# Optimization experiments

Hardware: AMD Instinct MI355X
Metric: run time of the kernel (lower is better)

## Reference

```python
import jax, jax.numpy as jnp
import numpy as np

B, N, C = 8, 4096, 512
H = 8
OUT = 512
DH = C // H  # 64
LN_EPS = 1e-5
L2_EPS = 1e-12


def setup_inputs() -> dict:
    key = jax.random.key(0)
    ks = jax.random.split(key, 6)
    x = jax.random.normal(ks[0], (B, N, C), dtype=jnp.float32)
    ln_g = jnp.ones((C,), dtype=jnp.float32)
    ln_b = jnp.zeros((C,), dtype=jnp.float32)
    qkv_w = jax.random.normal(ks[1], (3 * C, C), dtype=jnp.float32) * 0.02  # torch Linear weight [out,in]
    temperature = jnp.ones((H, 1, 1), dtype=jnp.float32)
    proj_w = jax.random.normal(ks[2], (OUT, C), dtype=jnp.float32) * 0.02
    proj_b = jnp.zeros((OUT,), dtype=jnp.float32)
    return {"x": x, "ln_g": ln_g, "ln_b": ln_b, "qkv_w": qkv_w,
            "temperature": temperature, "proj_w": proj_w, "proj_b": proj_b}


def reference(x, ln_g, ln_b, qkv_w, temperature, proj_w, proj_b):
    # LayerNorm
    mu = jnp.mean(x, axis=-1, keepdims=True)
    var = jnp.mean(jnp.square(x - mu), axis=-1, keepdims=True)
    xn = (x - mu) * jax.lax.rsqrt(var + LN_EPS) * ln_g + ln_b
    # QKV projection (no bias)
    qkv = xn @ qkv_w.T  # [B,N,3C]
    qkv = qkv.reshape(B, N, 3, H, DH).transpose(2, 0, 3, 4, 1)  # [3,B,H,DH,N]
    q, k, v = qkv[0], qkv[1], qkv[2]  # each [B,H,DH,N] (already 'transposed' channel layout)
    # L2-normalize q,k along token dim (matches F.normalize eps behavior)
    q = q / jnp.clip(jnp.linalg.norm(q, axis=-1, keepdims=True), L2_EPS)
    k = k / jnp.clip(jnp.linalg.norm(k, axis=-1, keepdims=True), L2_EPS)
    # channel attention [B,H,DH,DH], scaled by per-head temperature
    attn = jnp.einsum('bhdn,bhen->bhde', q, k) * temperature[None]
    attn = jax.nn.softmax(attn, axis=-1)
    out = jnp.einsum('bhde,bhen->bhdn', attn, v)  # [B,H,DH,N]
    out = out.transpose(0, 3, 1, 2).reshape(B, N, H * DH)  # [B,N,C]
    out = jax.nn.gelu(out, approximate=False)
    out = out @ proj_w.T + proj_b
    return out
```

## Files before the change

kernel.cpp:

```cpp
#include <hip/hip_runtime.h>
#include <hip/hip_bf16.h>

typedef __hip_bfloat16 bf16;
typedef __bf16 bfrag __attribute__((ext_vector_type(8)));
typedef float f32x4 __attribute__((ext_vector_type(4)));

#define AS1 __attribute__((address_space(1)))
#define AS3 __attribute__((address_space(3)))

static constexpr int Bb = 8, Nn = 4096, Cc = 512, Hh = 8;
static constexpr int Mtok = Bb * Nn;
static constexpr int QKVC = 3 * Cc;
static constexpr size_t WS_NEED = 57147392;

__device__ __forceinline__ void gl_lds16(const void* g, void* l) {
  __builtin_amdgcn_global_load_lds((const AS1 void*)g, (AS3 void*)l, 16, 0, 0);
}
__device__ __forceinline__ float gelu_exact(float x) {
  return 0.5f * x * (1.0f + erff(x * 0.70710678118654752f));
}

__global__ __launch_bounds__(256) void fill_f32(float* o, float val, int n) {
  int i = blockIdx.x * 256 + threadIdx.x;
  if (i < n) o[i] = val;
}

__global__ __launch_bounds__(256) void cvt_f32_bf16(const float* __restrict__ a,
                                                    bf16* __restrict__ o, int n) {
  int i = (blockIdx.x * 256 + threadIdx.x) * 8;
  if (i + 8 <= n) {
    float f[8];
    *(float4*)f       = *(const float4*)(a + i);
    *(float4*)(f + 4) = *(const float4*)(a + i + 4);
    bf16 v[8];
#pragma unroll
    for (int j = 0; j < 8; ++j) v[j] = __float2bfloat16(f[j]);
    *(uint4*)(o + i) = *(uint4*)v;
  }
}

__global__ __launch_bounds__(256) void ln_kernel(const float* __restrict__ x,
                                                 const float* __restrict__ gw,
                                                 const float* __restrict__ bw,
                                                 bf16* __restrict__ xn) {
  int tok  = blockIdx.x * 4 + (threadIdx.x >> 6);
  int lane = threadIdx.x & 63;
  const float* xr = x + (size_t)tok * Cc + lane * 8;
  float f[8];
  *(float4*)f       = *(const float4*)xr;
  *(float4*)(f + 4) = *(const float4*)(xr + 4);
  float s = 0.f;
#pragma unroll
  for (int j = 0; j < 8; ++j) s += f[j];
#pragma unroll
  for (int m = 32; m; m >>= 1) s += __shfl_xor(s, m);
  float mu = s * (1.0f / 512.0f);
  float q = 0.f;
#pragma unroll
  for (int j = 0; j < 8; ++j) { float d = f[j] - mu; q += d * d; }
#pragma unroll
  for (int m = 32; m; m >>= 1) q += __shfl_xor(q, m);
  float rstd = rsqrtf(q * (1.0f / 512.0f) + 1e-5f);
  bf16 o[8];
#pragma unroll
  for (int j = 0; j < 8; ++j)
    o[j] = __float2bfloat16((f[j] - mu) * rstd * gw[lane * 8 + j] + bw[lane * 8 + j]);
  *(uint4*)(xn + (size_t)tok * Cc + lane * 8) = *(uint4*)o;
}

template <typename TC>
__global__ __launch_bounds__(256) void gemm_bt(const bf16* __restrict__ A,
                                               const bf16* __restrict__ B,
                                               TC* __restrict__ C,
                                               int M, int N, int K,
                                               const float* __restrict__ bias,
                                               long sA_z, long sB_z, long sC_z) {
  A += (size_t)blockIdx.z * sA_z;
  B += (size_t)blockIdx.z * sB_z;
  C += (size_t)blockIdx.z * sC_z;
  __shared__ __align__(16) bf16 smem[16384];
  bf16* sA = smem;
  bf16* sB = smem + 8192;
  int t = threadIdx.x, w = t >> 6, lane = t & 63, fr = lane & 15, quad = lane >> 4;
  int n0 = blockIdx.x * 128, m0 = blockIdx.y * 128;
  int wm = (w >> 1) * 64, wn = (w & 1) * 64;
  f32x4 acc[4][4] = {};

  for (int k0 = 0; k0 < K; k0 += 64) {
    __syncthreads();
#pragma unroll
    for (int c2 = 0; c2 < 4; ++c2) {
      int c = w * 4 + c2;
      int row = c * 8 + (lane >> 3);
      int ke  = (lane & 7) * 8;
      gl_lds16(A + (size_t)(m0 + row) * K + k0 + ke, (char*)sA + c * 1024);
      gl_lds16(B + (size_t)(n0 + row) * K + k0 + ke, (char*)sB + c * 1024);
    }
    __syncthreads();
#pragma unroll
    for (int kk = 0; kk < 64; kk += 32) {
      bfrag af[4], bg[4];
#pragma unroll
      for (int i = 0; i < 4; ++i) af[i] = *(const bfrag*)(sA + (wm + i * 16 + fr) * 64 + kk + quad * 8);
#pragma unroll
      for (int j = 0; j < 4; ++j) bg[j] = *(const bfrag*)(sB + (wn + j * 16 + fr) * 64 + kk + quad * 8);
#pragma unroll
      for (int i = 0; i < 4; ++i)
#pragma unroll
        for (int j = 0; j < 4; ++j)
          acc[i][j] = __builtin_amdgcn_mfma_f32_16x16x32_bf16(af[i], bg[j], acc[i][j], 0, 0, 0);
    }
  }

  if constexpr (__is_same(TC, float)) {
#pragma unroll
    for (int j = 0; j < 4; ++j) {
      float bj = bias ? bias[n0 + wn + j * 16 + fr] : 0.0f;
#pragma unroll
      for (int i = 0; i < 4; ++i)
#pragma unroll
        for (int r = 0; r < 4; ++r)
          C[(size_t)(m0 + wm + i * 16 + quad * 4 + r) * N + n0 + wn + j * 16 + fr] =
              acc[i][j][r] + bj;
    }
  } else {
    __syncthreads();
    bf16* ct = smem;
#pragma unroll
    for (int j = 0; j < 4; ++j) {
      float bj = bias ? bias[n0 + wn + j * 16 + fr] : 0.0f;
#pragma unroll
      for (int i = 0; i < 4; ++i)
#pragma unroll
        for (int r = 0; r < 4; ++r)
          ct[(wm + i * 16 + quad * 4 + r) * 128 + wn + j * 16 + fr] =
              __float2bfloat16(acc[i][j][r] + bj);
    }
    __syncthreads();
#pragma unroll
    for (int r8 = 0; r8 < 8; ++r8) {
      int row = r8 * 16 + (t >> 4);
      int ce  = (t & 15) * 8;
      *(uint4*)(C + (size_t)(m0 + row) * N + n0 + ce) = *(const uint4*)(smem + row * 128 + ce);
    }
  }
}

__global__ __launch_bounds__(256) void xtx(const bf16* __restrict__ xn,
                                           float* __restrict__ Gcov) {
  int tile = blockIdx.x;
  int split = blockIdx.y;
  int b = blockIdx.z;
  int m0 = (tile >> 2) * 128, n0 = (tile & 3) * 128;
  int t = threadIdx.x, w = t >> 6, lane = t & 63, fr = lane & 15, quad = lane >> 4;
  int wm = (w >> 1) * 64, wn = (w & 1) * 64;
  __shared__ __align__(16) bf16 sA[8192], sB[8192];
  f32x4 acc[4][4] = {};
  const bf16* xb = xn + ((size_t)b * Nn + split * 512) * Cc;
  int ch0 = (t & 15) * 8;
  int tg  = t >> 4;
  unsigned swz = (unsigned)(t & 7);
  unsigned wpos = (((unsigned)(tg >> 1) ^ swz) * 16u) + (unsigned)(tg & 1) * 8u;
  uint4 va[4], vb[4];
#pragma unroll
  for (int j = 0; j < 4; ++j) {
    int tk = tg * 4 + j;
    va[j] = *(const uint4*)(xb + (size_t)tk * Cc + m0 + ch0);
    vb[j] = *(const uint4*)(xb + (size_t)tk * Cc + n0 + ch0);
  }
  for (int kc = 0; kc < 8; ++kc) {
    __syncthreads();
#pragma unroll
    for (int k = 0; k < 4; ++k) {
      unsigned a0 = ((const unsigned*)&va[0])[k], a1 = ((const unsigned*)&va[1])[k];
      unsigned a2 = ((const unsigned*)&va[2])[k], a3 = ((const unsigned*)&va[3])[k];
      uint2 lo = { (a0 & 0xffffu) | (a1 << 16), (a2 & 0xffffu) | (a3 << 16) };
      uint2 hi = { (a0 >> 16) | (a1 & 0xffff0000u), (a2 >> 16) | (a3 & 0xffff0000u) };
      *(uint2*)((char*)sA + (unsigned)(ch0 + 2 * k) * 128 + wpos) = lo;
      *(uint2*)((char*)sA + (unsigned)(ch0 + 2 * k + 1) * 128 + wpos) = hi;
      unsigned b0 = ((const unsigned*)&vb[0])[k], b1 = ((const unsigned*)&vb[1])[k];
      unsigned b2 = ((const unsigned*)&vb[2])[k], b3 = ((const unsigned*)&vb[3])[k];
      uint2 lo2 = { (b0 & 0xffffu) | (b1 << 16), (b2 & 0xffffu) | (b3 << 16) };
      uint2 hi2 = { (b0 >> 16) | (b1 & 0xffff0000u), (b2 >> 16) | (b3 & 0xffff0000u) };
      *(uint2*)((char*)sB + (unsigned)(ch0 + 2 * k) * 128 + wpos) = lo2;
      *(uint2*)((char*)sB + (unsigned)(ch0 + 2 * k + 1) * 128 + wpos) = hi2;
    }
    __syncthreads();
    if (kc < 7) {
      const bf16* xb2 = xb + (size_t)(kc + 1) * 64 * Cc;
#pragma unroll
      for (int j = 0; j < 4; ++j) {
        int tk = tg * 4 + j;
        va[j] = *(const uint4*)(xb2 + (size_t)tk * Cc + m0 + ch0);
        vb[j] = *(const uint4*)(xb2 + (size_t)tk * Cc + n0 + ch0);
      }
    }
#pragma unroll
    for (int s = 0; s < 2; ++s) {
      bfrag af[4], bg[4];
#pragma unroll
      for (int i = 0; i < 4; ++i) {
        int ch = wm + i * 16 + fr;
        int blk = (s * 4 + quad) ^ ((ch >> 3) & 7);
        af[i] = *(const bfrag*)(sA + ch * 64 + blk * 8);
      }
#pragma unroll
      for (int j = 0; j < 4; ++j) {
        int ch = wn + j * 16 + fr;
        int blk = (s * 4 + quad) ^ ((ch >> 3) & 7);
        bg[j] = *(const bfrag*)(sB + ch * 64 + blk * 8);
      }
#pragma unroll
      for (int i = 0; i < 4; ++i)
#pragma unroll
        for (int j = 0; j < 4; ++j)
          acc[i][j] = __builtin_amdgcn_mfma_f32_16x16x32_bf16(af[i], bg[j], acc[i][j], 0, 0, 0);
    }
  }
  float* gb = Gcov + (size_t)b * Cc * Cc;
#pragma unroll
  for (int i = 0; i < 4; ++i)
#pragma unroll
    for (int j = 0; j < 4; ++j)
#pragma unroll
      for (int r = 0; r < 4; ++r)
        atomicAdd(&gb[(size_t)(m0 + wm + i * 16 + quad * 4 + r) * Cc + n0 + wn + j * 16 + fr],
                  acc[i][j][r]);
}

__global__ __launch_bounds__(256) void gram_softmax(const bf16* __restrict__ T,
                                                    const bf16* __restrict__ wq,
                                                    const float* __restrict__ temp,
                                                    bf16* __restrict__ P) {
  int h = blockIdx.x, b = blockIdx.y;
  int t = threadIdx.x, w = t >> 6, lane = t & 63, fr = lane & 15, quad = lane >> 4;
  const bf16* Tq = T + (size_t)b * 1024 * 512 + (size_t)(h * 64) * 512;
  const bf16* Tk = T + (size_t)b * 1024 * 512 + (size_t)(512 + h * 64) * 512;
  const bf16* Wqh = wq + (size_t)(h * 64) * 512;
  const bf16* Wkh = wq + (size_t)(512 + h * 64) * 512;
  f32x4 acc[4][4] = {};
#pragma unroll
  for (int s = 0; s < 4; ++s) {
    int kb = w * 128 + s * 32 + quad * 8;
    bfrag af[4], bg[4];
#pragma unroll
    for (int i = 0; i < 4; ++i) af[i] = *(const bfrag*)(Tq + (size_t)(i * 16 + fr) * 512 + kb);
#pragma unroll
    for (int j = 0; j < 4; ++j) bg[j] = *(const bfrag*)(Wkh + (size_t)(j * 16 + fr) * 512 + kb);
#pragma unroll
    for (int i = 0; i < 4; ++i)
#pragma unroll
      for (int j = 0; j < 4; ++j)
        acc[i][j] = __builtin_amdgcn_mfma_f32_16x16x32_bf16(af[i], bg[j], acc[i][j], 0, 0, 0);
  }
  __shared__ float parts[4 * 4096];
  __shared__ float nrm[2][4][64];
  __shared__ float nqk[2][64];
#pragma unroll
  for (int i = 0; i < 4; ++i)
#pragma unroll
    for (int j = 0; j < 4; ++j)
#pragma unroll
      for (int r = 0; r < 4; ++r)
        parts[w * 4096 + (i * 16 + quad * 4 + r) * 64 + j * 16 + fr] = acc[i][j][r];
  {
    int d = t & 63, qtr = t >> 6, c0 = qtr * 128;
    float pq = 0.f, pk = 0.f;
#pragma unroll 4
    for (int cc = 0; cc < 16; ++cc) {
      bf16 a[8], ww[8];
      *(uint4*)a  = *(const uint4*)(Tq + (size_t)d * 512 + c0 + cc * 8);
      *(uint4*)ww = *(const uint4*)(Wqh + (size_t)d * 512 + c0 + cc * 8);
#pragma unroll
      for (int j = 0; j < 8; ++j) pq += __bfloat162float(a[j]) * __bfloat162float(ww[j]);
      *(uint4*)a  = *(const uint4*)(Tk + (size_t)d * 512 + c0 + cc * 8);
      *(uint4*)ww = *(const uint4*)(Wkh + (size_t)d * 512 + c0 + cc * 8);
#pragma unroll
      for (int j = 0; j < 8; ++j) pk += __bfloat162float(a[j]) * __bfloat162float(ww[j]);
    }
    nrm[0][qtr][d] = pq;
    nrm[1][qtr][d] = pk;
  }
  __syncthreads();
  if (t < 64) {
    nqk[0][t] = fmaxf(sqrtf(nrm[0][0][t] + nrm[0][1][t] + nrm[0][2][t] + nrm[0][3][t]), 1e-12f);
    nqk[1][t] = fmaxf(sqrtf(nrm[1][0][t] + nrm[1][1][t] + nrm[1][2][t] + nrm[1][3][t]), 1e-12f);
  }
  __syncthreads();
  if (t < 64) {
    int d = t;
    float sc = temp[h] / nqk[0][d];
    float l[64]; float mx = -1e30f;
#pragma unroll
    for (int e = 0; e < 64; ++e) {
      float vsum = parts[d * 64 + e] + parts[4096 + d * 64 + e] +
                   parts[8192 + d * 64 + e] + parts[12288 + d * 64 + e];
      l[e] = vsum * sc / nqk[1][e];
      mx = fmaxf(mx, l[e]);
    }
    float sum = 0.f;
#pragma unroll
    for (int e = 0; e < 64; ++e) { l[e] = expf(l[e] - mx); sum += l[e]; }
    float inv = 1.0f / sum;
    bf16* pr = P + ((size_t)(b * 8 + h) * 64 + d) * 64;
#pragma unroll
    for (int e = 0; e < 64; ++e) pr[e] = __float2bfloat16(l[e] * inv);
  }
}

__global__ __launch_bounds__(256) void pv_gelu(const bf16* __restrict__ P,
                                               const bf16* __restrict__ v,
                                               bf16* __restrict__ g) {
  int chunk = blockIdx.x, h = blockIdx.y, b = blockIdx.z;
  int t = threadIdx.x, w = t >> 6, lane = t & 63, fr = lane & 15, quad = lane >> 4;
  const bf16* pb = P + (size_t)(b * 8 + h) * 4096;
  bfrag pf[4][2];
#pragma unroll
  for (int i = 0; i < 4; ++i)
#pragma unroll
    for (int c = 0; c < 2; ++c)
      pf[i][c] = *(const bfrag*)(pb + (i * 16 + fr) * 64 + c * 32 + quad * 8);
#pragma unroll 2
  for (int nt = 0; nt < 8; ++nt) {
    int ntok = chunk * 512 + w * 128 + nt * 16 + fr;
    const bf16* vrow = v + (size_t)(b * Nn + ntok) * Cc + h * 64 + quad * 8;
    bfrag bv0 = *(const bfrag*)(vrow);
    bfrag bv1 = *(const bfrag*)(vrow + 32);
    f32x4 acc[4] = {};
#pragma unroll
    for (int i = 0; i < 4; ++i) {
      acc[i] = __builtin_amdgcn_mfma_f32_16x16x32_bf16(pf[i][0], bv0, acc[i], 0, 0, 0);
      acc[i] = __builtin_amdgcn_mfma_f32_16x16x32_bf16(pf[i][1], bv1, acc[i], 0, 0, 0);
    }
    bf16* grow = g + (size_t)(b * Nn + ntok) * Cc + h * 64;
#pragma unroll
    for (int i = 0; i < 4; ++i) {
      bf16 o[4];
#pragma unroll
      for (int r = 0; r < 4; ++r) o[r] = __float2bfloat16(gelu_exact(acc[i][r]));
      *(uint2*)(grow + i * 16 + quad * 4) = *(uint2*)o;
    }
  }
}

extern "C" void kernel_launch(void* const* d_in, const int* in_sizes, int n_in,
                              void* d_out, int out_size, void* d_ws, size_t ws_size,
                              hipStream_t stream) {
  const float* x      = (const float*)d_in[0];
  const float* ln_g   = (const float*)d_in[1];
  const float* ln_b   = (const float*)d_in[2];
  const float* qkv_w  = (const float*)d_in[3];
  const float* temp   = (const float*)d_in[4];
  const float* proj_w = (const float*)d_in[5];
  const float* proj_b = (const float*)d_in[6];
  float* out = (float*)d_out;
  char*  ws  = (char*)d_ws;

  const int exp_sizes[7] = {16777216, 512, 512, 786432, 8, 262144, 512};
  bool sizes_ok = (n_in == 7) && (out_size == 16777216);
  if (sizes_ok) for (int i = 0; i < 7; ++i) sizes_ok = sizes_ok && (in_sizes[i] == exp_sizes[i]);
  if (!sizes_ok) {
    fill_f32<<<(16777216 + 255) / 256, 256, 0, stream>>>(out, 500.0f, out_size);
    return;
  }
  if (ws_size < WS_NEED) {
    fill_f32<<<(16777216 + 255) / 256, 256, 0, stream>>>(out, (float)(ws_size >> 20), out_size);
    return;
  }

  bf16*  xn   = (bf16*)ws;
  bf16*  g    = (bf16*)ws;
  float* Gcov = (float*)(ws + 33554432);
  bf16*  Gcvb = (bf16*)(ws + 41943040);
  bf16*  T    = (bf16*)(ws + 46137344);
  bf16*  P    = (bf16*)(ws + 54525952);
  bf16*  wq   = (bf16*)(ws + 55050240);
  bf16*  wp   = (bf16*)(ws + 56623104);
  bf16*  v    = (bf16*)d_out;

  cvt_f32_bf16<<<384, 256, 0, stream>>>(qkv_w, wq, QKVC * Cc);
  cvt_f32_bf16<<<128, 256, 0, stream>>>(proj_w, wp, Cc * Cc);
  hipMemsetAsync(Gcov, 0, (size_t)Bb * Cc * Cc * sizeof(float), stream);
  ln_kernel<<<Mtok / 4, 256, 0, stream>>>(x, ln_g, ln_b, xn);
  gemm_bt<bf16><<<dim3(4, 256, 1), 256, 0, stream>>>(xn, wq + 1024 * 512, v, Mtok, Cc, Cc,
                                                     nullptr, 0, 0, 0);
  xtx<<<dim3(16, 8, 8), 256, 0, stream>>>(xn, Gcov);
  cvt_f32_bf16<<<1024, 256, 0, stream>>>(Gcov, Gcvb, Bb * Cc * Cc);
  gemm_bt<bf16><<<dim3(4, 8, 8), 256, 0, stream>>>(wq, Gcvb, T, 1024, Cc, Cc,
                                                   nullptr, 0, (long)Cc * Cc, (long)1024 * Cc);
  gram_softmax<<<dim3(Hh, Bb), 256, 0, stream>>>(T, wq, temp, P);
  pv_gelu<<<dim3(8, Hh, Bb), 256, 0, stream>>>(P, v, g);
  gemm_bt<float><<<dim3(4, 256, 1), 256, 0, stream>>>(g, wp, out, Mtok, Cc, Cc,
                                                      proj_b, 0, 0, 0);
}
```

Measured before the change: 316.1 us.

## Exploit Gram matrix symmetry: compute upper-triangle tiles only, mirror during conversion

Result: faster. 291.1 us (-7.9%).

```diff
diff --git a/kernel.cpp b/kernel.cpp
--- a/kernel.cpp
+++ b/kernel.cpp
@@ -19,6 +19,7 @@
 __device__ __forceinline__ float gelu_exact(float x) {
   return 0.5f * x * (1.0f + erff(x * 0.70710678118654752f));
 }
+__device__ __forceinline__ int g3(int x) { return ((x & 1) << 2) | (x >> 1); }
 
 __global__ __launch_bounds__(256) void fill_f32(float* o, float val, int n) {
   int i = blockIdx.x * 256 + threadIdx.x;
@@ -36,6 +37,52 @@
 #pragma unroll
     for (int j = 0; j < 8; ++j) v[j] = __float2bfloat16(f[j]);
     *(uint4*)(o + i) = *(uint4*)v;
+  }
+}
+
+__global__ __launch_bounds__(256) void cvt_mirror(const float* __restrict__ Gcov,
+                                                  bf16* __restrict__ Gcvb) {
+  int tile = blockIdx.x, b = blockIdx.y;
+  int ti = tile >> 2, tj = tile & 3;
+  int t = threadIdx.x;
+  const float* gb = Gcov + (size_t)b * Cc * Cc;
+  bf16* ob = Gcvb + (size_t)b * Cc * Cc;
+  if (ti <= tj) {
+#pragma unroll
+    for (int r8 = 0; r8 < 8; ++r8) {
+      int row = r8 * 16 + (t >> 4), col = (t & 15) * 8;
+      const float* src = gb + (size_t)(ti * 128 + row) * Cc + tj * 128 + col;
+      float f[8];
+      *(float4*)f       = *(const float4*)src;
+      *(float4*)(f + 4) = *(const float4*)(src + 4);
+      bf16 v[8];
+#pragma unroll
+      for (int j = 0; j < 8; ++j) v[j] = __float2bfloat16(f[j]);
+      *(uint4*)(ob + (size_t)(ti * 128 + row) * Cc + tj * 128 + col) = *(uint4*)v;
+    }
+  } else {
+    __shared__ bf16 ls[128][136];
+#pragma unroll
+    for (int r8 = 0; r8 < 8; ++r8) {
+      int srow = r8 * 16 + (t >> 4), scol = (t & 15) * 8;
+      const float* src = gb + (size_t)(tj * 128 + srow) * Cc + ti * 128 + scol;
+      float f[8];
+      *(float4*)f       = *(const float4*)src;
+      *(float4*)(f + 4) = *(const float4*)(src + 4);
+      bf16 v[8];
+#pragma unroll
+      for (int j = 0; j < 8; ++j) v[j] = __float2bfloat16(f[j]);
+      *(uint4*)&ls[srow][scol] = *(uint4*)v;
+    }
+    __syncthreads();
+#pragma unroll
+    for (int r8 = 0; r8 < 8; ++r8) {
+      int orow = r8 * 16 + (t >> 4), ocol = (t & 15) * 8;
+      bf16 v[8];
+#pragma unroll
+      for (int u = 0; u < 8; ++u) v[u] = ls[ocol + u][orow];
+      *(uint4*)(ob + (size_t)(ti * 128 + orow) * Cc + tj * 128 + ocol) = *(uint4*)v;
+    }
   }
 }
 
@@ -148,25 +195,31 @@
 
 __global__ __launch_bounds__(256) void xtx(const bf16* __restrict__ xn,
                                            float* __restrict__ Gcov) {
-  int tile = blockIdx.x;
-  int split = blockIdx.y;
-  int b = blockIdx.z;
-  int m0 = (tile >> 2) * 128, n0 = (tile & 3) * 128;
+  int flat = blockIdx.x;
+  int idx  = (flat & 7) * 80 + (flat >> 3);
+  int tile = idx % 10;
+  int sb   = idx / 10;
+  int split = sb & 7, b = sb >> 3;
+  int tm = tile < 4 ? 0 : tile < 7 ? 1 : tile < 9 ? 2 : 3;
+  int tn = tile < 4 ? tile : tile < 7 ? tile - 3 : tile < 9 ? tile - 5 : 3;
+  int m0 = tm * 128, n0 = tn * 128;
+  bool diag = (m0 == n0);
   int t = threadIdx.x, w = t >> 6, lane = t & 63, fr = lane & 15, quad = lane >> 4;
   int wm = (w >> 1) * 64, wn = (w & 1) * 64;
   __shared__ __align__(16) bf16 sA[8192], sB[8192];
+  const bf16* sBp = diag ? sA : sB;
   f32x4 acc[4][4] = {};
   const bf16* xb = xn + ((size_t)b * Nn + split * 512) * Cc;
   int ch0 = (t & 15) * 8;
   int tg  = t >> 4;
-  unsigned swz = (unsigned)(t & 7);
-  unsigned wpos = (((unsigned)(tg >> 1) ^ swz) * 16u) + (unsigned)(tg & 1) * 8u;
+  int swz = g3(t & 7);
+  unsigned wpos = (((unsigned)((tg >> 1) ^ swz)) * 16u) + (unsigned)(tg & 1) * 8u;
   uint4 va[4], vb[4];
 #pragma unroll
   for (int j = 0; j < 4; ++j) {
     int tk = tg * 4 + j;
     va[j] = *(const uint4*)(xb + (size_t)tk * Cc + m0 + ch0);
-    vb[j] = *(const uint4*)(xb + (size_t)tk * Cc + n0 + ch0);
+    if (!diag) vb[j] = *(const uint4*)(xb + (size_t)tk * Cc + n0 + ch0);
   }
   for (int kc = 0; kc < 8; ++kc) {
     __syncthreads();
@@ -178,12 +231,14 @@
       uint2 hi = { (a0 >> 16) | (a1 & 0xffff0000u), (a2 >> 16) | (a3 & 0xffff0000u) };
       *(uint2*)((char*)sA + (unsigned)(ch0 + 2 * k) * 128 + wpos) = lo;
       *(uint2*)((char*)sA + (unsigned)(ch0 + 2 * k + 1) * 128 + wpos) = hi;
-      unsigned b0 = ((const unsigned*)&vb[0])[k], b1 = ((const unsigned*)&vb[1])[k];
-      unsigned b2 = ((const unsigned*)&vb[2])[k], b3 = ((const unsigned*)&vb[3])[k];
-      uint2 lo2 = { (b0 & 0xffffu) | (b1 << 16), (b2 & 0xffffu) | (b3 << 16) };
-      uint2 hi2 = { (b0 >> 16) | (b1 & 0xffff0000u), (b2 >> 16) | (b3 & 0xffff0000u) };
-      *(uint2*)((char*)sB + (unsigned)(ch0 + 2 * k) * 128 + wpos) = lo2;
-      *(uint2*)((char*)sB + (unsigned)(ch0 + 2 * k + 1) * 128 + wpos) = hi2;
+      if (!diag) {
+        unsigned b0 = ((const unsigned*)&vb[0])[k], b1 = ((const unsigned*)&vb[1])[k];
+        unsigned b2 = ((const unsigned*)&vb[2])[k], b3 = ((const unsigned*)&vb[3])[k];
+        uint2 lo2 = { (b0 & 0xffffu) | (b1 << 16), (b2 & 0xffffu) | (b3 << 16) };
+        uint2 hi2 = { (b0 >> 16) | (b1 & 0xffff0000u), (b2 >> 16) | (b3 & 0xffff0000u) };
+        *(uint2*)((char*)sB + (unsigned)(ch0 + 2 * k) * 128 + wpos) = lo2;
+        *(uint2*)((char*)sB + (unsigned)(ch0 + 2 * k + 1) * 128 + wpos) = hi2;
+      }
     }
     __syncthreads();
     if (kc < 7) {
@@ -192,7 +247,7 @@
       for (int j = 0; j < 4; ++j) {
         int tk = tg * 4 + j;
         va[j] = *(const uint4*)(xb2 + (size_t)tk * Cc + m0 + ch0);
-        vb[j] = *(const uint4*)(xb2 + (size_t)tk * Cc + n0 + ch0);
+        if (!diag) vb[j] = *(const uint4*)(xb2 + (size_t)tk * Cc + n0 + ch0);
       }
     }
 #pragma unroll
@@ -201,14 +256,14 @@
 #pragma unroll
       for (int i = 0; i < 4; ++i) {
         int ch = wm + i * 16 + fr;
-        int blk = (s * 4 + quad) ^ ((ch >> 3) & 7);
+        int blk = (s * 4 + quad) ^ g3((ch >> 3) & 7);
         af[i] = *(const bfrag*)(sA + ch * 64 + blk * 8);
       }
 #pragma unroll
       for (int j = 0; j < 4; ++j) {
         int ch = wn + j * 16 + fr;
-        int blk = (s * 4 + quad) ^ ((ch >> 3) & 7);
-        bg[j] = *(const bfrag*)(sB + ch * 64 + blk * 8);
+        int blk = (s * 4 + quad) ^ g3((ch >> 3) & 7);
+        bg[j] = *(const bfrag*)(sBp + ch * 64 + blk * 8);
       }
 #pragma unroll
       for (int i = 0; i < 4; ++i)
@@ -384,8 +439,8 @@
   ln_kernel<<<Mtok / 4, 256, 0, stream>>>(x, ln_g, ln_b, xn);
   gemm_bt<bf16><<<dim3(4, 256, 1), 256, 0, stream>>>(xn, wq + 1024 * 512, v, Mtok, Cc, Cc,
                                                      nullptr, 0, 0, 0);
-  xtx<<<dim3(16, 8, 8), 256, 0, stream>>>(xn, Gcov);
-  cvt_f32_bf16<<<1024, 256, 0, stream>>>(Gcov, Gcvb, Bb * Cc * Cc);
+  xtx<<<640, 256, 0, stream>>>(xn, Gcov);
+  cvt_mirror<<<dim3(16, 8), 256, 0, stream>>>(Gcov, Gcvb);
   gemm_bt<bf16><<<dim3(4, 8, 8), 256, 0, stream>>>(wq, Gcvb, T, 1024, Cc, Cc,
                                                    nullptr, 0, (long)Cc * Cc, (long)1024 * Cc);
   gram_softmax<<<dim3(Hh, Bb), 256, 0, stream>>>(T, wq, temp, P);
```
